# Kernel tuning notes

Hardware: AMD Instinct MI355X
Metric: run time of the kernel (lower is better)

The kernel has to match this reference:

```python
import jax, jax.numpy as jnp
import numpy as np

DIM = 1024
HEADS = 16
HEAD_DIM = DIM // HEADS
ROPE_BASE = 500000.0
SCALE = HEAD_DIM ** -0.5


def _rope_cos_sin(T, dtype=jnp.float32):
    inv_freq = 1.0 / (ROPE_BASE ** (jnp.arange(0, HEAD_DIM, 2, dtype=jnp.float32) / HEAD_DIM))
    t = jnp.arange(T, dtype=jnp.float32)
    freqs = t[:, None] * inv_freq[None, :]            # (T, hd/2)
    emb = jnp.concatenate([freqs, freqs], axis=-1)    # (T, hd)
    return jnp.cos(emb).astype(dtype), jnp.sin(emb).astype(dtype)


def _rotate_half(x):
    x1, x2 = jnp.split(x, 2, axis=-1)
    return jnp.concatenate([-x2, x1], axis=-1)


def _apply_rope(x, cos, sin):
    # x: (B,H,T,hd); cos/sin: (T,hd)
    return x * cos + _rotate_half(x) * sin


def setup_inputs() -> dict:
    key = jax.random.key(0)
    k1, k2, k3 = jax.random.split(key, 3)
    B, T = 4, 4096
    x = jax.random.normal(k1, (B, T, DIM), dtype=jnp.float32)
    W_qkv = jax.random.normal(k2, (DIM, 3 * DIM), dtype=jnp.float32) * (DIM ** -0.5)
    W_out = jax.random.normal(k3, (DIM, DIM), dtype=jnp.float32) * (DIM ** -0.5)
    return {"x": x, "W_qkv": W_qkv, "W_out": W_out}


def reference(x, W_qkv, W_out):
    B, T, D = x.shape
    H, hd = HEADS, HEAD_DIM
    qkv = (x @ W_qkv).reshape(B, T, 3, H, hd).transpose(2, 0, 3, 1, 4)  # (3,B,H,T,hd)
    q, k, v = qkv[0], qkv[1], qkv[2]
    cos, sin = _rope_cos_sin(T, q.dtype)
    q = _apply_rope(q, cos, sin)
    k = _apply_rope(k, cos, sin)
    # linear attention: elu+1 feature map
    q_feat = jax.nn.elu(q * SCALE) + 1.0
    k_feat = jax.nn.elu(k) + 1.0
    kv = jnp.einsum('bhtd,bhtv->bhdv', k_feat, v)      # (B,H,hd,hd)
    k_sum = k_feat.sum(axis=2)                          # (B,H,hd)
    denom = jnp.maximum(jnp.einsum('bhtd,bhd->bht', q_feat, k_sum), 1e-6)
    out = jnp.einsum('bhtd,bhdv->bhtv', q_feat, kv) / denom[..., None]
    out = out.transpose(0, 2, 1, 3).reshape(B, T, D)
    return out @ W_out
```

## Files before the change

### kernel.cpp

```cpp
#include <hip/hip_runtime.h>
#include <hip/hip_bf16.h>

typedef __bf16 bf16;
typedef bf16 bf16x4 __attribute__((ext_vector_type(4)));
typedef bf16 bf16x8 __attribute__((ext_vector_type(8)));
typedef float f32x4 __attribute__((ext_vector_type(4)));

#define GLD_LDS16(gptr, lptr) \
  __builtin_amdgcn_global_load_lds((const __attribute__((address_space(1))) unsigned int*)(gptr), \
                                   (__attribute__((address_space(3))) unsigned int*)(lptr), 16, 0, 0)

__global__ __launch_bounds__(256) void f32_to_bf16(const float* __restrict__ in,
                                                   bf16* __restrict__ out) {
  const size_t i = ((size_t)blockIdx.x * 256 + threadIdx.x) * 8;
  float4 a = *(const float4*)(in + i);
  float4 b = *(const float4*)(in + i + 4);
  bf16x8 o;
  o[0] = (bf16)a.x; o[1] = (bf16)a.y; o[2] = (bf16)a.z; o[3] = (bf16)a.w;
  o[4] = (bf16)b.x; o[5] = (bf16)b.y; o[6] = (bf16)b.z; o[7] = (bf16)b.w;
  *(bf16x8*)(out + i) = o;
}

__global__ __launch_bounds__(256) void prep(const float* __restrict__ Wqkv,
                                            const float* __restrict__ Wout,
                                            bf16* __restrict__ WqkvT,
                                            bf16* __restrict__ WoutT,
                                            float2* __restrict__ ctab) {
  const int bid = blockIdx.x;
  if (bid < 512) {
    const int idx = bid * 256 + threadIdx.x;
    const int t = idx >> 5, f = idx & 31;
    const float invf = (float)exp(-((double)f / 32.0) * log(500000.0));
    float sn, cs;
    sincosf((float)t * invf, &sn, &cs);
    ctab[idx] = make_float2(cs, sn);
    return;
  }
  __shared__ float tile[32][33];
  const float* in;
  bf16* out;
  int R, C, bx, by;
  if (bid < 3584) {
    const int t = bid - 512;
    in = Wqkv; out = WqkvT; R = 1024; C = 3072;
    bx = (t % 96) * 32; by = (t / 96) * 32;
  } else {
    const int t = bid - 3584;
    in = Wout; out = WoutT; R = 1024; C = 1024;
    bx = (t & 31) * 32; by = (t >> 5) * 32;
  }
  const int tx = threadIdx.x & 31;
  const int ty = threadIdx.x >> 5;
#pragma unroll
  for (int i = 0; i < 4; i++)
    tile[ty + i * 8][tx] = in[(size_t)(by + ty + i * 8) * C + bx + tx];
  __syncthreads();
#pragma unroll
  for (int i = 0; i < 4; i++)
    out[(size_t)(bx + ty + i * 8) * R + by + tx] = (bf16)tile[tx][ty + i * 8];
}

__device__ __forceinline__ void gemm256_core(const bf16* __restrict__ A,
                                             const bf16* __restrict__ BT,
                                             const int K, const int m0, const int n0,
                                             bf16* __restrict__ As, bf16* __restrict__ Bs,
                                             f32x4 acc[8][4]) {
  const int tid = threadIdx.x;
  const int lane = tid & 63;
  const int w = tid >> 6;
  const int wm = w >> 2, wn = w & 3;

#pragma unroll
  for (int i = 0; i < 8; i++)
#pragma unroll
    for (int j = 0; j < 4; j++) acc[i][j] = f32x4{0.f, 0.f, 0.f, 0.f};

  const int lch = (tid & 3) ^ ((tid >> 3) & 3);
  const bf16* Ag = A + (size_t)(m0 + (tid >> 2)) * K + lch * 8;
  const bf16* Bg = BT + (size_t)(n0 + (tid >> 2)) * K + lch * 8;
  const int wb = w * 512;

#define STG(kh, db, k0)                                                   \
  do {                                                                    \
    bf16* aD = As + ((db) * 2 + (kh)) * 8192 + wb;                        \
    bf16* bD = Bs + ((db) * 2 + (kh)) * 8192 + wb;                        \
    const size_t go = (size_t)(k0) + (kh) * 32;                           \
    GLD_LDS16(Ag + go, aD);                                               \
    GLD_LDS16(Ag + (size_t)128 * K + go, aD + 4096);                      \
    GLD_LDS16(Bg + go, bD);                                               \
    GLD_LDS16(Bg + (size_t)128 * K + go, bD + 4096);                      \
  } while (0)

  const int fr = lane & 15;
  const int kq = lane >> 4;
  const int frow = fr * 32 + ((kq ^ ((fr >> 1) & 3)) << 3);
  const int aro = wm * 4096;
  const int bro = wn * 2048;

#define LOADFRAGS(kh, db)                                                 \
  const bf16* Ap = As + ((db) * 2 + (kh)) * 8192 + aro + frow;            \
  const bf16* Bp = Bs + ((db) * 2 + (kh)) * 8192 + bro + frow;            \
  bf16x8 af[8], bv[4];                                                    \
  _Pragma("unroll") for (int mi = 0; mi < 8; mi++)                        \
      af[mi] = *(const bf16x8*)(Ap + mi * 512);                           \
  _Pragma("unroll") for (int ni = 0; ni < 4; ni++)                        \
      bv[ni] = *(const bf16x8*)(Bp + ni * 512);

#define MFMA32                                                            \
  __builtin_amdgcn_s_setprio(1);                                          \
  _Pragma("unroll") for (int mi = 0; mi < 8; mi++)                        \
  _Pragma("unroll") for (int ni = 0; ni < 4; ni++)                        \
      acc[mi][ni] = __builtin_amdgcn_mfma_f32_16x16x32_bf16(              \
          af[mi], bv[ni], acc[mi][ni], 0, 0, 0);                          \
  __builtin_amdgcn_s_setprio(0);

  STG(0, 0, 0);
  STG(1, 0, 0);
  if (K > 64) {
    STG(0, 1, 64);
    asm volatile("s_waitcnt vmcnt(8)" ::: "memory");
  } else {
    asm volatile("s_waitcnt vmcnt(4)" ::: "memory");
  }
  __builtin_amdgcn_s_barrier();

  const int NT = K >> 6;
  for (int kt = 0; kt < NT; ++kt) {
    const int db = kt & 1;
    {
      LOADFRAGS(0, db);
      if (kt + 1 < NT) STG(1, db ^ 1, (kt + 1) * 64);
      __builtin_amdgcn_s_barrier();
      asm volatile("s_waitcnt lgkmcnt(0)" ::: "memory");
      __builtin_amdgcn_sched_barrier(0);
      MFMA32;
      if (kt + 1 < NT) asm volatile("s_waitcnt vmcnt(8)" ::: "memory");
      else             asm volatile("s_waitcnt vmcnt(0)" ::: "memory");
      __builtin_amdgcn_s_barrier();
    }
    {
      LOADFRAGS(1, db);
      if (kt + 2 < NT) STG(0, db, (kt + 2) * 64);
      __builtin_amdgcn_s_barrier();
      asm volatile("s_waitcnt lgkmcnt(0)" ::: "memory");
      __builtin_amdgcn_sched_barrier(0);
      MFMA32;
      if (kt + 2 < NT)      asm volatile("s_waitcnt vmcnt(8)" ::: "memory");
      else if (kt + 1 < NT) asm volatile("s_waitcnt vmcnt(4)" ::: "memory");
      __builtin_amdgcn_s_barrier();
    }
  }
#undef STG
#undef LOADFRAGS
#undef MFMA32
}

__device__ __forceinline__ void xcd_tile(int& m0, int& n0) {
  const int gx = gridDim.x;
  const int nwg = gx * gridDim.y;
  const int orig = blockIdx.y * gx + blockIdx.x;
  const int cpx = nwg >> 3;
  const int swb = (orig & 7) * cpx + (orig >> 3);
  m0 = (swb / gx) * 256;
  n0 = (swb % gx) * 256;
}

__global__ __launch_bounds__(512, 2) void gemm_qkv_fused(const bf16* __restrict__ A,
                                                         const bf16* __restrict__ BT,
                                                         const float2* __restrict__ ctab,
                                                         bf16* __restrict__ qfB,
                                                         bf16* __restrict__ kfT,
                                                         bf16* __restrict__ vfT) {
  __shared__ __attribute__((aligned(16))) bf16 As[32768];
  __shared__ __attribute__((aligned(16))) bf16 Bs[32768];
  const int K = 1024;
  int m0, n0;
  xcd_tile(m0, n0);

  f32x4 acc[8][4];
  gemm256_core(A, BT, K, m0, n0, As, Bs, acc);

  const int lane = threadIdx.x & 63;
  const int w = threadIdx.x >> 6;
  const int wm = w >> 2, wn = w & 3;
  const int fr15 = lane & 15;
  const int cb = n0 + wn * 64;
  const int p = cb >> 10;
  const int hh = (cb & 1023) >> 6;
  const int row00 = m0 + wm * 128 + ((lane >> 4) << 2);
  const int b = row00 >> 12;
  const size_t base0 = ((size_t)(b * 16 + hh)) * 4096 * 64;
  const int tb = row00 & 4095;

  if (p == 2) {
#pragma unroll
    for (int mi = 0; mi < 8; mi++)
#pragma unroll
      for (int ni = 0; ni < 4; ni++) {
        bf16x4 o;
#pragma unroll
        for (int r = 0; r < 4; r++) o[r] = (bf16)acc[mi][ni][r];
        *(bf16x4*)(vfT + base0 + (size_t)(fr15 + ni * 16) * 4096 + tb + mi * 16) = o;
      }
  } else if (p == 1) {
#pragma unroll
    for (int mi = 0; mi < 8; mi++)
#pragma unroll
      for (int ni = 0; ni < 2; ni++) {
        bf16x4 olo, ohi;
#pragma unroll
        for (int r = 0; r < 4; r++) {
          const int tloc = tb + mi * 16 + r;
          const float2 cs2 = ctab[tloc * 32 + fr15 + ni * 16];
          const float x1 = acc[mi][ni][r], x2 = acc[mi][ni + 2][r];
          const float r1 = x1 * cs2.x - x2 * cs2.y;
          const float r2 = x2 * cs2.x + x1 * cs2.y;
          olo[r] = (bf16)(r1 > 0.f ? r1 + 1.f : __expf(r1));
          ohi[r] = (bf16)(r2 > 0.f ? r2 + 1.f : __expf(r2));
        }
        bf16* dp = kfT + base0 + (size_t)(fr15 + ni * 16) * 4096 + tb + mi * 16;
        *(bf16x4*)dp = olo;
        *(bf16x4*)(dp + (size_t)32 * 4096) = ohi;
      }
  } else {
#pragma unroll
    for (int mi = 0; mi < 8; mi++)
#pragma unroll
      for (int r = 0; r < 4; r++) {
        const int tloc = tb + mi * 16 + r;
        const float2* ct = ctab + tloc * 32;
        bf16* dst = qfB + base0 + (size_t)tloc * 64;
#pragma unroll
        for (int ni = 0; ni < 2; ni++) {
          const float2 cs2 = ct[fr15 + ni * 16];
          const float x1 = acc[mi][ni][r], x2 = acc[mi][ni + 2][r];
          const float r1 = (x1 * cs2.x - x2 * cs2.y) * 0.125f;
          const float r2 = (x2 * cs2.x + x1 * cs2.y) * 0.125f;
          dst[fr15 + ni * 16] = (bf16)(r1 > 0.f ? r1 + 1.f : __expf(r1));
          dst[fr15 + ni * 16 + 32] = (bf16)(r2 > 0.f ? r2 + 1.f : __expf(r2));
        }
      }
  }
}

__global__ __launch_bounds__(512, 2) void gemm_bt_f32(const bf16* __restrict__ A,
                                                      const bf16* __restrict__ BT,
                                                      float* __restrict__ C,
                                                      int N, int K) {
  __shared__ __attribute__((aligned(16))) bf16 As[32768];
  __shared__ __attribute__((aligned(16))) bf16 Bs[32768];
  int m0, n0;
  xcd_tile(m0, n0);

  f32x4 acc[8][4];
  gemm256_core(A, BT, K, m0, n0, As, Bs, acc);

  const int lane = threadIdx.x & 63;
  const int w = threadIdx.x >> 6;
  const int wm = w >> 2, wn = w & 3;
  const int col0 = n0 + wn * 64 + (lane & 15);
  const int row00 = m0 + wm * 128 + ((lane >> 4) << 2);
#pragma unroll
  for (int mi = 0; mi < 8; mi++)
#pragma unroll
    for (int ni = 0; ni < 4; ni++)
#pragma unroll
      for (int r = 0; r < 4; r++)
        C[(size_t)(row00 + mi * 16 + r) * N + col0 + ni * 16] = acc[mi][ni][r];
}

__global__ __launch_bounds__(256) void attn_kv_mfma(const bf16* __restrict__ kfT,
                                                    const bf16* __restrict__ vfT,
                                                    float* __restrict__ kvg,
                                                    float* __restrict__ ksumg) {
  const int bh = blockIdx.x;
  const int kc = blockIdx.y;
  const int tid = threadIdx.x;
  const int lane = tid & 63;
  const int w = tid >> 6;
  const int fr = lane & 15;
  const int kq = lane >> 4;

  __shared__ __attribute__((aligned(16))) float kvp[4][64][68];

  const size_t hb = (size_t)bh * 64 * 4096;
  const int kbase = kc * 512 + w * 128 + kq * 8;

  f32x4 acc[4][4];
#pragma unroll
  for (int i = 0; i < 4; i++)
#pragma unroll
    for (int j = 0; j < 4; j++) acc[i][j] = f32x4{0.f, 0.f, 0.f, 0.f};
  float ks[4] = {0.f, 0.f, 0.f, 0.f};

#pragma unroll
  for (int c = 0; c < 4; c++) {
    const int k0 = kbase + c * 32;
    bf16x8 af[4], bv[4];
#pragma unroll
    for (int mi = 0; mi < 4; mi++)
      af[mi] = *(const bf16x8*)(kfT + hb + (size_t)(mi * 16 + fr) * 4096 + k0);
#pragma unroll
    for (int ni = 0; ni < 4; ni++)
      bv[ni] = *(const bf16x8*)(vfT + hb + (size_t)(ni * 16 + fr) * 4096 + k0);
#pragma unroll
    for (int mi = 0; mi < 4; mi++) {
#pragma unroll
      for (int ni = 0; ni < 4; ni++)
        acc[mi][ni] = __builtin_amdgcn_mfma_f32_16x16x32_bf16(af[mi], bv[ni], acc[mi][ni], 0, 0, 0);
#pragma unroll
      for (int e = 0; e < 8; e++) ks[mi] += (float)af[mi][e];
    }
  }

#pragma unroll
  for (int mi = 0; mi < 4; mi++) {
    ks[mi] += __shfl_xor(ks[mi], 16, 64);
    ks[mi] += __shfl_xor(ks[mi], 32, 64);
  }
  if (kq == 0) {
#pragma unroll
    for (int mi = 0; mi < 4; mi++)
      atomicAdd(&ksumg[bh * 64 + mi * 16 + fr], ks[mi]);
  }

#pragma unroll
  for (int mi = 0; mi < 4; mi++)
#pragma unroll
    for (int ni = 0; ni < 4; ni++)
#pragma unroll
      for (int r = 0; r < 4; r++)
        kvp[w][mi * 16 + kq * 4 + r][ni * 16 + fr] = acc[mi][ni][r];
  __syncthreads();

  const int d = tid >> 2;
  const int v0 = (tid & 3) * 16;
#pragma unroll
  for (int j = 0; j < 16; j++) {
    const float s = kvp[0][d][v0 + j] + kvp[1][d][v0 + j] +
                    kvp[2][d][v0 + j] + kvp[3][d][v0 + j];
    atomicAdd(&kvg[(size_t)bh * 4096 + d * 64 + v0 + j], s);
  }
}

__global__ __launch_bounds__(256) void attn_out(const bf16* __restrict__ qfB,
                                                const float* __restrict__ kvg,
                                                const float* __restrict__ ksumg,
                                                bf16* __restrict__ attn) {
  const int bh = blockIdx.y;
  const int b = bh >> 4, h = bh & 15;
  const int t0 = blockIdx.x * 256;
  __shared__ __attribute__((aligned(16))) float qf[64][68];
  __shared__ __attribute__((aligned(16))) float kvs[64][64];
  __shared__ __attribute__((aligned(16))) float ksums[64];
  const int tid = threadIdx.x;

#pragma unroll
  for (int j = 0; j < 4; j++) {
    int idx = tid + 256 * j;
    *(float4*)&kvs[idx >> 4][(idx & 15) * 4] = *(const float4*)&kvg[(size_t)bh * 4096 + idx * 4];
  }
  if (tid < 64) ksums[tid] = ksumg[bh * 64 + tid];

  const int tr = tid >> 4, cc = tid & 15;

  for (int sub = 0; sub < 4; sub++) {
    if (sub) __syncthreads();
    const int ts = t0 + sub * 64;
#pragma unroll
    for (int j = 0; j < 2; j++) {
      int chunk = tid + 256 * j;
      int tl = chunk >> 3, col = (chunk & 7) * 8;
      bf16x8 r = *(const bf16x8*)(qfB + ((size_t)bh * 4096 + ts + tl) * 64 + col);
      f32x4 a, bb;
#pragma unroll
      for (int q = 0; q < 4; q++) { a[q] = (float)r[q]; bb[q] = (float)r[q + 4]; }
      *(f32x4*)&qf[tl][col] = a;
      *(f32x4*)&qf[tl][col + 4] = bb;
    }
    __syncthreads();

    f32x4 acc[4];
#pragma unroll
    for (int r = 0; r < 4; r++) acc[r] = f32x4{0.f, 0.f, 0.f, 0.f};
    f32x4 dn = f32x4{0.f, 0.f, 0.f, 0.f};

    for (int d2 = 0; d2 < 64; d2++) {
      f32x4 kv4 = *(const f32x4*)&kvs[d2][cc * 4];
      float kss = ksums[d2];
#pragma unroll
      for (int r = 0; r < 4; r++) {
        float qv = qf[tr * 4 + r][d2];
        acc[r] += qv * kv4;
        dn[r] += qv * kss;
      }
    }

#pragma unroll
    for (int r = 0; r < 4; r++) {
      const float rdn = 1.f / fmaxf(dn[r], 1e-6f);
      bf16x4 o;
#pragma unroll
      for (int c = 0; c < 4; c++) o[c] = (bf16)(acc[r][c] * rdn);
      *(bf16x4*)(attn + ((size_t)(b * 4096) + ts + tr * 4 + r) * 1024 + h * 64 + cc * 4) = o;
    }
  }
}

extern "C" void kernel_launch(void* const* d_in, const int* in_sizes, int n_in,
                              void* d_out, int out_size, void* d_ws, size_t ws_size,
                              hipStream_t stream) {
  if (ws_size < 177225728ULL) return;

  const float* x = (const float*)d_in[0];
  const float* Wqkv = (const float*)d_in[1];
  const float* Wout = (const float*)d_in[2];
  float* out = (float*)d_out;
  char* ws = (char*)d_ws;

  float* kvg = (float*)(ws);
  float* ksumg = (float*)(ws + 1048576);
  bf16* WqkvT = (bf16*)(ws + 1064960);
  bf16* WoutT = (bf16*)(ws + 7356416);
  bf16* attn = (bf16*)(ws + 9453568);
  float2* ctab = (float2*)(ws + 9453568);
  bf16* qfB = (bf16*)(ws + 43008000);
  bf16* kfT = (bf16*)(ws + 76562432);
  bf16* vfT = (bf16*)(ws + 110116864);
  bf16* xB = (bf16*)(ws + 143671296);

  hipMemsetAsync(ws, 0, 1048576 + 16384, stream);

  prep<<<4608, 256, 0, stream>>>(Wqkv, Wout, WqkvT, WoutT, ctab);
  f32_to_bf16<<<16777216 / (256 * 8), 256, 0, stream>>>(x, xB);

  gemm_qkv_fused<<<dim3(3072 / 256, 16384 / 256), 512, 0, stream>>>(xB, WqkvT, ctab, qfB, kfT, vfT);

  attn_kv_mfma<<<dim3(64, 8), 256, 0, stream>>>(kfT, vfT, kvg, ksumg);
  attn_out<<<dim3(16, 64), 256, 0, stream>>>(qfB, kvg, ksumg, attn);

  gemm_bt_f32<<<dim3(1024 / 256, 16384 / 256), 512, 0, stream>>>(attn, WoutT, out, 1024, 1024);
}
```

Measured before the change: 438.7 us.

## Merge x conversion into prep, stage KV tiles via LDS, widen attention grids

```diff
diff --git a/kernel.cpp b/kernel.cpp
--- a/kernel.cpp
+++ b/kernel.cpp
@@ -10,23 +10,24 @@
   __builtin_amdgcn_global_load_lds((const __attribute__((address_space(1))) unsigned int*)(gptr), \
                                    (__attribute__((address_space(3))) unsigned int*)(lptr), 16, 0, 0)
 
-__global__ __launch_bounds__(256) void f32_to_bf16(const float* __restrict__ in,
-                                                   bf16* __restrict__ out) {
-  const size_t i = ((size_t)blockIdx.x * 256 + threadIdx.x) * 8;
-  float4 a = *(const float4*)(in + i);
-  float4 b = *(const float4*)(in + i + 4);
-  bf16x8 o;
-  o[0] = (bf16)a.x; o[1] = (bf16)a.y; o[2] = (bf16)a.z; o[3] = (bf16)a.w;
-  o[4] = (bf16)b.x; o[5] = (bf16)b.y; o[6] = (bf16)b.z; o[7] = (bf16)b.w;
-  *(bf16x8*)(out + i) = o;
-}
-
 __global__ __launch_bounds__(256) void prep(const float* __restrict__ Wqkv,
                                             const float* __restrict__ Wout,
+                                            const float* __restrict__ x,
                                             bf16* __restrict__ WqkvT,
                                             bf16* __restrict__ WoutT,
+                                            bf16* __restrict__ xB,
                                             float2* __restrict__ ctab) {
   const int bid = blockIdx.x;
+  if (bid >= 4608) {
+    const size_t i = ((size_t)(bid - 4608) * 256 + threadIdx.x) * 8;
+    float4 a = *(const float4*)(x + i);
+    float4 b = *(const float4*)(x + i + 4);
+    bf16x8 o;
+    o[0] = (bf16)a.x; o[1] = (bf16)a.y; o[2] = (bf16)a.z; o[3] = (bf16)a.w;
+    o[4] = (bf16)b.x; o[5] = (bf16)b.y; o[6] = (bf16)b.z; o[7] = (bf16)b.w;
+    *(bf16x8*)(xB + i) = o;
+    return;
+  }
   if (bid < 512) {
     const int idx = bid * 256 + threadIdx.x;
     const int t = idx >> 5, f = idx & 31;
@@ -273,6 +274,10 @@
                                                     const bf16* __restrict__ vfT,
                                                     float* __restrict__ kvg,
                                                     float* __restrict__ ksumg) {
+  __shared__ __attribute__((aligned(16))) bf16 sh[2 * 64 * 128];
+  bf16* Ksh = sh;
+  bf16* Vsh = sh + 64 * 128;
+
   const int bh = blockIdx.x;
   const int kc = blockIdx.y;
   const int tid = threadIdx.x;
@@ -280,11 +285,8 @@
   const int w = tid >> 6;
   const int fr = lane & 15;
   const int kq = lane >> 4;
-
-  __shared__ __attribute__((aligned(16))) float kvp[4][64][68];
-
   const size_t hb = (size_t)bh * 64 * 4096;
-  const int kbase = kc * 512 + w * 128 + kq * 8;
+  const int t0 = kc * 256;
 
   f32x4 acc[4][4];
 #pragma unroll
@@ -293,16 +295,28 @@
     for (int j = 0; j < 4; j++) acc[i][j] = f32x4{0.f, 0.f, 0.f, 0.f};
   float ks[4] = {0.f, 0.f, 0.f, 0.f};
 
-#pragma unroll
-  for (int c = 0; c < 4; c++) {
-    const int k0 = kbase + c * 32;
+  const int fswz = ((w * 4 + kq) ^ (fr & 7)) << 3;
+
+  for (int rnd = 0; rnd < 2; rnd++) {
+    if (rnd) __syncthreads();
+    const int tb = t0 + rnd * 128;
+#pragma unroll
+    for (int i = 0; i < 4; i++) {
+      const int row = w * 16 + i * 4 + (lane >> 4);
+      const int lc = (lane & 15) ^ (row & 7);
+      const size_t src = hb + (size_t)row * 4096 + tb + lc * 8;
+      GLD_LDS16(kfT + src, Ksh + (w * 16 + i * 4) * 128);
+      GLD_LDS16(vfT + src, Vsh + (w * 16 + i * 4) * 128);
+    }
+    __syncthreads();
+
     bf16x8 af[4], bv[4];
 #pragma unroll
     for (int mi = 0; mi < 4; mi++)
-      af[mi] = *(const bf16x8*)(kfT + hb + (size_t)(mi * 16 + fr) * 4096 + k0);
+      af[mi] = *(const bf16x8*)(Ksh + (mi * 16 + fr) * 128 + fswz);
 #pragma unroll
     for (int ni = 0; ni < 4; ni++)
-      bv[ni] = *(const bf16x8*)(vfT + hb + (size_t)(ni * 16 + fr) * 4096 + k0);
+      bv[ni] = *(const bf16x8*)(Vsh + (ni * 16 + fr) * 128 + fswz);
 #pragma unroll
     for (int mi = 0; mi < 4; mi++) {
 #pragma unroll
@@ -324,22 +338,22 @@
       atomicAdd(&ksumg[bh * 64 + mi * 16 + fr], ks[mi]);
   }
 
+  __syncthreads();
+  float* kvs = (float*)sh;
+  for (int i = tid; i < 64 * 65; i += 256) kvs[i] = 0.f;
+  __syncthreads();
 #pragma unroll
   for (int mi = 0; mi < 4; mi++)
 #pragma unroll
     for (int ni = 0; ni < 4; ni++)
 #pragma unroll
       for (int r = 0; r < 4; r++)
-        kvp[w][mi * 16 + kq * 4 + r][ni * 16 + fr] = acc[mi][ni][r];
+        atomicAdd(&kvs[(mi * 16 + kq * 4 + r) * 65 + ni * 16 + fr], acc[mi][ni][r]);
   __syncthreads();
-
-  const int d = tid >> 2;
-  const int v0 = (tid & 3) * 16;
 #pragma unroll
   for (int j = 0; j < 16; j++) {
-    const float s = kvp[0][d][v0 + j] + kvp[1][d][v0 + j] +
-                    kvp[2][d][v0 + j] + kvp[3][d][v0 + j];
-    atomicAdd(&kvg[(size_t)bh * 4096 + d * 64 + v0 + j], s);
+    const int idx = tid + 256 * j;
+    atomicAdd(&kvg[(size_t)bh * 4096 + idx], kvs[(idx >> 6) * 65 + (idx & 63)]);
   }
 }
 
@@ -349,61 +363,55 @@
                                                 bf16* __restrict__ attn) {
   const int bh = blockIdx.y;
   const int b = bh >> 4, h = bh & 15;
-  const int t0 = blockIdx.x * 256;
+  const int t0 = blockIdx.x * 64;
   __shared__ __attribute__((aligned(16))) float qf[64][68];
   __shared__ __attribute__((aligned(16))) float kvs[64][64];
   __shared__ __attribute__((aligned(16))) float ksums[64];
   const int tid = threadIdx.x;
 
 #pragma unroll
+  for (int j = 0; j < 2; j++) {
+    int chunk = tid + 256 * j;
+    int tl = chunk >> 3, col = (chunk & 7) * 8;
+    bf16x8 r = *(const bf16x8*)(qfB + ((size_t)bh * 4096 + t0 + tl) * 64 + col);
+    f32x4 a, bb;
+#pragma unroll
+    for (int q = 0; q < 4; q++) { a[q] = (float)r[q]; bb[q] = (float)r[q + 4]; }
+    *(f32x4*)&qf[tl][col] = a;
+    *(f32x4*)&qf[tl][col + 4] = bb;
+  }
+#pragma unroll
   for (int j = 0; j < 4; j++) {
     int idx = tid + 256 * j;
     *(float4*)&kvs[idx >> 4][(idx & 15) * 4] = *(const float4*)&kvg[(size_t)bh * 4096 + idx * 4];
   }
   if (tid < 64) ksums[tid] = ksumg[bh * 64 + tid];
+  __syncthreads();
 
   const int tr = tid >> 4, cc = tid & 15;
-
-  for (int sub = 0; sub < 4; sub++) {
-    if (sub) __syncthreads();
-    const int ts = t0 + sub * 64;
-#pragma unroll
-    for (int j = 0; j < 2; j++) {
-      int chunk = tid + 256 * j;
-      int tl = chunk >> 3, col = (chunk & 7) * 8;
-      bf16x8 r = *(const bf16x8*)(qfB + ((size_t)bh * 4096 + ts + tl) * 64 + col);
-      f32x4 a, bb;
-#pragma unroll
-      for (int q = 0; q < 4; q++) { a[q] = (float)r[q]; bb[q] = (float)r[q + 4]; }
-      *(f32x4*)&qf[tl][col] = a;
-      *(f32x4*)&qf[tl][col + 4] = bb;
+  f32x4 acc[4];
+#pragma unroll
+  for (int r = 0; r < 4; r++) acc[r] = f32x4{0.f, 0.f, 0.f, 0.f};
+  f32x4 dn = f32x4{0.f, 0.f, 0.f, 0.f};
+
+  for (int d2 = 0; d2 < 64; d2++) {
+    f32x4 kv4 = *(const f32x4*)&kvs[d2][cc * 4];
+    float ksv = ksums[d2];
+#pragma unroll
+    for (int r = 0; r < 4; r++) {
+      float qv = qf[tr * 4 + r][d2];
+      acc[r] += qv * kv4;
+      dn[r] += qv * ksv;
     }
-    __syncthreads();
-
-    f32x4 acc[4];
-#pragma unroll
-    for (int r = 0; r < 4; r++) acc[r] = f32x4{0.f, 0.f, 0.f, 0.f};
-    f32x4 dn = f32x4{0.f, 0.f, 0.f, 0.f};
-
-    for (int d2 = 0; d2 < 64; d2++) {
-      f32x4 kv4 = *(const f32x4*)&kvs[d2][cc * 4];
-      float kss = ksums[d2];
-#pragma unroll
-      for (int r = 0; r < 4; r++) {
-        float qv = qf[tr * 4 + r][d2];
-        acc[r] += qv * kv4;
-        dn[r] += qv * kss;
-      }
-    }
-
-#pragma unroll
-    for (int r = 0; r < 4; r++) {
-      const float rdn = 1.f / fmaxf(dn[r], 1e-6f);
-      bf16x4 o;
-#pragma unroll
-      for (int c = 0; c < 4; c++) o[c] = (bf16)(acc[r][c] * rdn);
-      *(bf16x4*)(attn + ((size_t)(b * 4096) + ts + tr * 4 + r) * 1024 + h * 64 + cc * 4) = o;
-    }
+  }
+
+#pragma unroll
+  for (int r = 0; r < 4; r++) {
+    const float rdn = 1.f / fmaxf(dn[r], 1e-6f);
+    bf16x4 o;
+#pragma unroll
+    for (int c = 0; c < 4; c++) o[c] = (bf16)(acc[r][c] * rdn);
+    *(bf16x4*)(attn + ((size_t)(b * 4096) + t0 + tr * 4 + r) * 1024 + h * 64 + cc * 4) = o;
   }
 }
 
@@ -431,13 +439,12 @@
 
   hipMemsetAsync(ws, 0, 1048576 + 16384, stream);
 
-  prep<<<4608, 256, 0, stream>>>(Wqkv, Wout, WqkvT, WoutT, ctab);
-  f32_to_bf16<<<16777216 / (256 * 8), 256, 0, stream>>>(x, xB);
+  prep<<<12800, 256, 0, stream>>>(Wqkv, Wout, x, WqkvT, WoutT, xB, ctab);
 
   gemm_qkv_fused<<<dim3(3072 / 256, 16384 / 256), 512, 0, stream>>>(xB, WqkvT, ctab, qfB, kfT, vfT);
 
-  attn_kv_mfma<<<dim3(64, 8), 256, 0, stream>>>(kfT, vfT, kvg, ksumg);
-  attn_out<<<dim3(16, 64), 256, 0, stream>>>(qfB, kvg, ksumg, attn);
+  attn_kv_mfma<<<dim3(64, 16), 256, 0, stream>>>(kfT, vfT, kvg, ksumg);
+  attn_out<<<dim3(64, 64), 256, 0, stream>>>(qfB, kvg, ksumg, attn);
 
   gemm_bt_f32<<<dim3(1024 / 256, 16384 / 256), 512, 0, stream>>>(attn, WoutT, out, 1024, 1024);
 }
```

Measured after the change: 414.7 us. 5.5% less time.
